# Kernel tuning notes

Hardware: AMD Instinct MI355X
Metric: run time of the kernel (lower is better)

## Reference

```python
import jax, jax.numpy as jnp
import numpy as np

N, NFEAT, NHID1, NHID2 = 16384, 128, 128, 64

def setup_inputs() -> dict:
    key = jax.random.key(0)
    k1, k2, k3, k4 = jax.random.split(key, 4)
    feature = jax.random.normal(k1, (N, NFEAT), dtype=jnp.float32)
    # dense (row-normalized) adjacency surrogate
    adj = jax.random.uniform(k2, (N, N), dtype=jnp.float32) / N
    W1 = jax.random.normal(k3, (NFEAT, NHID1), dtype=jnp.float32) / np.sqrt(NFEAT)
    b1 = jnp.zeros((NHID1,), dtype=jnp.float32)
    W2 = jax.random.normal(k4, (NHID1, NHID2), dtype=jnp.float32) / np.sqrt(NHID1)
    b2 = jnp.zeros((NHID2,), dtype=jnp.float32)
    return {"feature": feature, "adj": adj, "W1": W1, "b1": b1, "W2": W2, "b2": b2}

def reference(feature, adj, W1, b1, W2, b2):
    # layer 1: support = X@W1; agg = A@support; relu
    h = jax.nn.relu(adj @ (feature @ W1) + b1)
    # dropout is identity in eval mode
    # layer 2
    out = adj @ (h @ W2) + b2
    return out
```

## Files before the change

### kernel.cpp

```cpp
#include <hip/hip_runtime.h>
#include <stdint.h>

typedef float  f32x4  __attribute__((ext_vector_type(4)));
typedef short  short8 __attribute__((ext_vector_type(8)));
typedef __bf16 bf16x8 __attribute__((ext_vector_type(8)));

__device__ __forceinline__ unsigned short f2bf(float f) {
    unsigned u = __builtin_bit_cast(unsigned, f);
    unsigned r = u + 0x7fffu + ((u >> 16) & 1u);
    return (unsigned short)(r >> 16);
}

__device__ __forceinline__ short8 cvt8(f32x4 a, f32x4 b) {
    short8 r;
    r[0] = (short)f2bf(a[0]); r[1] = (short)f2bf(a[1]);
    r[2] = (short)f2bf(a[2]); r[3] = (short)f2bf(a[3]);
    r[4] = (short)f2bf(b[0]); r[5] = (short)f2bf(b[1]);
    r[6] = (short)f2bf(b[2]); r[7] = (short)f2bf(b[3]);
    return r;
}

typedef const __attribute__((address_space(1))) void* gas_p;
typedef __attribute__((address_space(3))) void*       las_p;
__device__ __forceinline__ void gld_lds16(const void* g, void* l) {
    __builtin_amdgcn_global_load_lds((gas_p)g, (las_p)l, 16, 0, 0);
}

__device__ __forceinline__ f32x4 mfma16(short8 a, short8 b, f32x4 c) {
    return __builtin_amdgcn_mfma_f32_16x16x32_bf16(
        __builtin_bit_cast(bf16x8, a), __builtin_bit_cast(bf16x8, b), c, 0, 0, 0);
}

template<int NMAT>
__global__ __launch_bounds__(256) void k_xw_t(const float* __restrict__ X,
                                              const float* __restrict__ W,
                                              short* __restrict__ St, int M) {
    constexpr int K   = 128;
    constexpr int NPT = NMAT / 4;
    __shared__ float Xs[64][129];
    __shared__ float Ws[K][NMAT];

    const int tid = threadIdx.x;
    const int m0  = blockIdx.x * 64;

    constexpr int WCH = K * NMAT / 4 / 256;
    #pragma unroll
    for (int j = 0; j < WCH; ++j) {
        int ch = tid + j * 256;
        ((float4*)Ws)[ch] = ((const float4*)W)[ch];
    }
    #pragma unroll
    for (int j = 0; j < 8; ++j) {
        int ch = tid + j * 256;
        int r = ch >> 5, c4 = ch & 31;
        float4 v = *(const float4*)(X + (size_t)(m0 + r) * K + c4 * 4);
        Xs[r][c4 * 4 + 0] = v.x; Xs[r][c4 * 4 + 1] = v.y;
        Xs[r][c4 * 4 + 2] = v.z; Xs[r][c4 * 4 + 3] = v.w;
    }
    __syncthreads();

    const int m  = tid & 63;
    const int n0 = (tid >> 6) * NPT;
    float acc[NPT];
    #pragma unroll
    for (int i = 0; i < NPT; ++i) acc[i] = 0.f;

    for (int k = 0; k < K; ++k) {
        float x = Xs[m][k];
        #pragma unroll
        for (int i = 0; i < NPT; i += 4) {
            float4 w = *(const float4*)&Ws[k][n0 + i];
            acc[i + 0] += x * w.x; acc[i + 1] += x * w.y;
            acc[i + 2] += x * w.z; acc[i + 3] += x * w.w;
        }
    }
    #pragma unroll
    for (int i = 0; i < NPT; ++i)
        St[(size_t)(n0 + i) * M + m0 + m] = (short)f2bf(acc[i]);
}

template<int BN, bool RELU>
__global__ __launch_bounds__(256, 2) void k_adj_gemm(const float* __restrict__ A,
                                                     const short* __restrict__ Bt,
                                                     const float* __restrict__ bias,
                                                     float* __restrict__ out,
                                                     int M, int K) {
    constexpr int BM    = 32, BK = 64;
    constexpr int NF    = BN / 32;
    constexpr int ACH   = BM * BK * 4 / (256 * 16);
    constexpr int BCH   = BN * BK * 2 / (256 * 16);
    constexpr int VMCNT = ACH + BCH;

    __shared__ float As[2][BM * 64];
    __shared__ short Bs[2][BN * 64];

    const int tid  = threadIdx.x;
    const int wave = tid >> 6, lane = tid & 63;
    const int lr   = lane & 15, lk = lane >> 4;
    const int wr   = wave >> 1, wc = wave & 1;
    const int row0 = blockIdx.x * BM;
    const int cbB  = wc * (BN / 2) * 128;
    const int key  = (lr & 7) << 4;

    const int aRow   = (wr * 16 + lr) * 256;
    const int aO0    = (lk * 32) ^ key,       aO0b = (lk * 32 + 16) ^ key;
    const int aO1    = (128 + lk * 32) ^ key, aO1b = (128 + lk * 32 + 16) ^ key;
    const int offs0  = (lk * 16) ^ key;
    const int offs1  = (64 + lk * 16) ^ key;

    f32x4 acc[NF];
    #pragma unroll
    for (int n = 0; n < NF; ++n) acc[n] = (f32x4)0.f;

    const int NT = K / BK;

#define STAGE_AB(BUF, KT)                                                       \
    {                                                                           \
        _Pragma("unroll")                                                       \
        for (int j = 0; j < ACH; ++j) {                                         \
            int o = (tid + j * 256) * 16;          \
            int r = o >> 8, w = o & 255;                                        \
            const char* src = (const char*)A + (size_t)(row0 + r) * K * 4       \
                              + (size_t)(KT) * 256 + (w ^ ((r & 7) << 4));      \
            gld_lds16(src, (char*)&As[BUF][0] + o);                             \
        }                                                                       \
        _Pragma("unroll")                                                       \
        for (int j = 0; j < BCH; ++j) {                                         \
            int o = (tid + j * 256) * 16;          \
            int r = o >> 7, w = o & 127;                                        \
            const char* src = (const char*)Bt + (size_t)r * (K * 2)             \
                              + (size_t)(KT) * 128 + (w ^ ((r & 7) << 4));      \
            gld_lds16(src, (char*)&Bs[BUF][0] + o);                             \
        }                                                                       \
    }

    STAGE_AB(0, 0)

#define ITER(KT, CUR, NXT)                                                      \
    {                                                                           \
             \
        { int ktn = (KT) + 1 < NT ? (KT) + 1 : NT - 1; STAGE_AB(NXT, ktn) }     \
        __builtin_amdgcn_sched_barrier(0);                                      \
        \
        asm volatile("s_waitcnt vmcnt(%0)" :: "i"(VMCNT) : "memory");           \
        __builtin_amdgcn_s_barrier();                                           \
        __builtin_amdgcn_sched_barrier(0);                                      \
                                      \
        const char* Ab = (const char*)&As[CUR][0] + aRow;                       \
        f32x4 A0a = *(const f32x4*)(Ab + aO0);                                  \
        f32x4 A0b = *(const f32x4*)(Ab + aO0b);                                 \
        f32x4 A1a = *(const f32x4*)(Ab + aO1);                                  \
        f32x4 A1b = *(const f32x4*)(Ab + aO1b);                                 \
        short8 fa0 = cvt8(A0a, A0b);                                            \
        short8 fa1 = cvt8(A1a, A1b);                                            \
                          \
        _Pragma("unroll")                                                       \
        for (int n = 0; n < NF; ++n) {                                          \
            short8 b0 = *(const short8*)((const char*)&Bs[CUR][0]               \
                                         + cbB + n * 2048 + lr * 128 + offs0);  \
            acc[n] = mfma16(fa0, b0, acc[n]);                                   \
            short8 b1 = *(const short8*)((const char*)&Bs[CUR][0]               \
                                         + cbB + n * 2048 + lr * 128 + offs1);  \
            acc[n] = mfma16(fa1, b1, acc[n]);                                   \
        }                                                                       \
        __builtin_amdgcn_sched_barrier(0);                                      \
        __builtin_amdgcn_s_barrier();         \
    }

    for (int g = 0; g < NT / 2; ++g) {
        ITER(2 * g,     0, 1)
        ITER(2 * g + 1, 1, 0)
    }
#undef ITER
#undef STAGE_AB

    #pragma unroll
    for (int n = 0; n < NF; ++n) {
        int col = wc * (BN / 2) + n * 16 + lr;
        float bv = bias[col];
        #pragma unroll
        for (int j = 0; j < 4; ++j) {
            int row = row0 + wr * 16 + lk * 4 + j;
            float v = acc[n][j] + bv;
            if (RELU) v = fmaxf(v, 0.f);
            out[(size_t)row * BN + col] = v;
        }
    }
}

extern "C" void kernel_launch(void* const* d_in, const int* in_sizes, int n_in,
                              void* d_out, int out_size, void* d_ws, size_t ws_size,
                              hipStream_t stream) {
    const int N = 16384, NH1 = 128, NH2 = 64;
    const float* feature = (const float*)d_in[0];
    const float* adj     = (const float*)d_in[1];
    const float* W1      = (const float*)d_in[2];
    const float* b1      = (const float*)d_in[3];
    const float* W2      = (const float*)d_in[4];
    const float* b2      = (const float*)d_in[5];

    short* S1t = (short*)d_ws;
    float* h   = (float*)((char*)d_ws + (4u << 20));
    short* S2t = (short*)((char*)d_ws + (12u << 20));

    k_xw_t<NH1><<<N / 64, 256, 0, stream>>>(feature, W1, S1t, N);
    k_adj_gemm<NH1, true ><<<N / 32, 256, 0, stream>>>(adj, S1t, b1, h, N, N);
    k_xw_t<NH2><<<N / 64, 256, 0, stream>>>(h, W2, S2t, N);
    k_adj_gemm<NH2, false><<<N / 32, 256, 0, stream>>>(adj, S2t, b2, (float*)d_out, N, N);
    (void)in_sizes; (void)n_in; (void)out_size; (void)ws_size;
}
```

Before: 577.9 us.

## Prefetch adjacency tiles two stages ahead with quad-buffered A in LDS

Splits the combined A/B staging into separate loads and quadruple-buffers the fp32 adjacency tile so it is issued two k-steps ahead, while the bf16 B tile stays one step ahead. The vmcnt wait is relaxed so more global loads stay in flight and latency on the bandwidth-dominant adjacency stream is better hidden. This doubles the A shared-memory footprint, which may lower occupancy, and the loop now requires NT to be divisible by 4.

```diff
diff --git a/kernel.cpp b/kernel.cpp
--- a/kernel.cpp
+++ b/kernel.cpp
@@ -89,9 +89,9 @@
     constexpr int NF    = BN / 32;
     constexpr int ACH   = BM * BK * 4 / (256 * 16);
     constexpr int BCH   = BN * BK * 2 / (256 * 16);
-    constexpr int VMCNT = ACH + BCH;
-
-    __shared__ float As[2][BM * 64];
+    constexpr int VMCNT = BCH + 2 * ACH;
+
+    __shared__ float As[4][BM * 64];
     __shared__ short Bs[2][BN * 64];
 
     const int tid  = threadIdx.x;
@@ -114,7 +114,7 @@
 
     const int NT = K / BK;
 
-#define STAGE_AB(BUF, KT)                                                       \
+#define STAGE_A(BUF, KT)                                                        \
     {                                                                           \
         _Pragma("unroll")                                                       \
         for (int j = 0; j < ACH; ++j) {                                         \
@@ -124,6 +124,9 @@
                               + (size_t)(KT) * 256 + (w ^ ((r & 7) << 4));      \
             gld_lds16(src, (char*)&As[BUF][0] + o);                             \
         }                                                                       \
+    }
+#define STAGE_B(BUF, KT)                                                        \
+    {                                                                           \
         _Pragma("unroll")                                                       \
         for (int j = 0; j < BCH; ++j) {                                         \
             int o = (tid + j * 256) * 16;          \
@@ -134,19 +137,22 @@
         }                                                                       \
     }
 
-    STAGE_AB(0, 0)
-
-#define ITER(KT, CUR, NXT)                                                      \
+    STAGE_A(0, 0)
+    STAGE_B(0, 0)
+    STAGE_A(1, 1)
+
+#define ITER(KT, CA, NA, CB, NB)                                                \
     {                                                                           \
-             \
-        { int ktn = (KT) + 1 < NT ? (KT) + 1 : NT - 1; STAGE_AB(NXT, ktn) }     \
+          \
+        { int ktn = (KT) + 1 < NT ? (KT) + 1 : NT - 1; STAGE_B(NB, ktn) }       \
+        { int kta = (KT) + 2 < NT ? (KT) + 2 : NT - 1; STAGE_A(NA, kta) }       \
         __builtin_amdgcn_sched_barrier(0);                                      \
-        \
+                         \
         asm volatile("s_waitcnt vmcnt(%0)" :: "i"(VMCNT) : "memory");           \
         __builtin_amdgcn_s_barrier();                                           \
         __builtin_amdgcn_sched_barrier(0);                                      \
                                       \
-        const char* Ab = (const char*)&As[CUR][0] + aRow;                       \
+        const char* Ab = (const char*)&As[CA][0] + aRow;                        \
         f32x4 A0a = *(const f32x4*)(Ab + aO0);                                  \
         f32x4 A0b = *(const f32x4*)(Ab + aO0b);                                 \
         f32x4 A1a = *(const f32x4*)(Ab + aO1);                                  \
@@ -156,23 +162,26 @@
                           \
         _Pragma("unroll")                                                       \
         for (int n = 0; n < NF; ++n) {                                          \
-            short8 b0 = *(const short8*)((const char*)&Bs[CUR][0]               \
+            short8 b0 = *(const short8*)((const char*)&Bs[CB][0]                \
                                          + cbB + n * 2048 + lr * 128 + offs0);  \
             acc[n] = mfma16(fa0, b0, acc[n]);                                   \
-            short8 b1 = *(const short8*)((const char*)&Bs[CUR][0]               \
+            short8 b1 = *(const short8*)((const char*)&Bs[CB][0]                \
                                          + cbB + n * 2048 + lr * 128 + offs1);  \
             acc[n] = mfma16(fa1, b1, acc[n]);                                   \
         }                                                                       \
         __builtin_amdgcn_sched_barrier(0);                                      \
-        __builtin_amdgcn_s_barrier();         \
-    }
-
-    for (int g = 0; g < NT / 2; ++g) {
-        ITER(2 * g,     0, 1)
-        ITER(2 * g + 1, 1, 0)
+        __builtin_amdgcn_s_barrier();        \
+    }
+
+    for (int g = 0; g < NT / 4; ++g) {
+        ITER(4 * g + 0, 0, 2, 0, 1)
+        ITER(4 * g + 1, 1, 3, 1, 0)
+        ITER(4 * g + 2, 2, 0, 0, 1)
+        ITER(4 * g + 3, 3, 1, 1, 0)
     }
 #undef ITER
-#undef STAGE_AB
+#undef STAGE_A
+#undef STAGE_B
 
     #pragma unroll
     for (int n = 0; n < NF; ++n) {
```

Measured after the change: 533.9 us. 7.6% less time.
